# Optimization experiments

Measured on AMD Instinct MI355X. Metric: run time of the kernel, lower is better.

Reference implementation:

```python
import jax, jax.numpy as jnp
import numpy as np

KERNEL_SIZE = 32
KERNEL_STRIDE = 16
HEAD_NUM_K = 4
HEAD_DIM = 128
BATCH = 4
SEQ_LEN = 16384


def _calc_chunks_with_stride(cu_seqlens_np, chunk_size, stride):
    """Mirror of calc_chunks_with_stride using numpy (index computation on host).

    Returns flat gather indices (num_chunks*chunk_size,) and compressed
    cumulative sequence lengths (batch+1,).
    """
    cu = np.asarray(cu_seqlens_np, dtype=np.int64)
    batch_sizes = cu[1:] - cu[:-1]
    max_seq_len = int(batch_sizes.max())
    max_chunks = max((max_seq_len - chunk_size) // stride + 1, 0)
    offsets = np.arange(0, max_chunks * stride, stride, dtype=np.int64)  # (C,)
    seq_starts = cu[:-1]
    chunk_start = seq_starts[:, None] + offsets[None, :]            # (B, C)
    chunk_end = chunk_start + chunk_size
    valid = chunk_end <= (seq_starts[:, None] + batch_sizes[:, None])  # (B, C)
    valid_starts = chunk_start[valid]                               # (N,)
    inner = np.arange(chunk_size, dtype=np.int64)[None, :]          # (1, K)
    flat_idx = (valid_starts[:, None] + inner).reshape(-1)          # (N*K,)
    n_per_batch = valid.sum(axis=1)
    cu_comp = np.zeros(len(cu), dtype=np.int32)
    cu_comp[1:] = np.cumsum(n_per_batch)
    return flat_idx, cu_comp


def setup_inputs() -> dict:
    key = jax.random.key(0)
    k = jax.random.normal(key, (BATCH * SEQ_LEN, HEAD_NUM_K, HEAD_DIM), dtype=jnp.float32)
    cu_seqlens = jnp.arange(BATCH + 1, dtype=jnp.int32) * SEQ_LEN
    return {"k": k, "cu_seqlens": cu_seqlens}


def reference(k, cu_seqlens):
    # Index computation is data-dependent on concrete cu_seqlens (host-side).
    flat_idx, cu_comp = _calc_chunks_with_stride(np.asarray(cu_seqlens), KERNEL_SIZE, KERNEL_STRIDE)
    idx = jnp.asarray(flat_idx)
    # Gather overlapping chunks: (N*K, H, D) -> (N, K, H, D) -> mean over K.
    gathered = k[idx]
    gathered = gathered.reshape(-1, KERNEL_SIZE, HEAD_NUM_K, HEAD_DIM)
    compressed_k = gathered.mean(axis=1)
    return compressed_k, jnp.asarray(cu_comp)
```

## Files before the change

kernel.cpp:

```cpp
#include <hip/hip_runtime.h>

#define KSIZE   32
#define KSTRIDE 16
#define HK      4
#define HD      128
#define ROW     (HK * HD)
#define ROW4    (ROW / 4)
#define BATCH   4
#define SEQLEN  16384
#define CHUNKS_PER_BATCH ((SEQLEN - KSIZE) / KSTRIDE + 1)
#define TOTAL_CHUNKS     (BATCH * CHUNKS_PER_BATCH)

#define SPAN 8
#define BLOCKS_PER_BATCH ((CHUNKS_PER_BATCH + SPAN - 1) / SPAN)
#define TOTAL_BLOCKS     (BATCH * BLOCKS_PER_BATCH)

__device__ __forceinline__ float4 sum16(const float4* __restrict__ src,
                                        int row0, int t) {
    float4 a0 = make_float4(0.f, 0.f, 0.f, 0.f);
    float4 a1 = make_float4(0.f, 0.f, 0.f, 0.f);
    #pragma unroll
    for (int i = 0; i < 8; ++i) {
        float4 u = src[(long)(row0 + 2 * i)     * ROW4 + t];
        float4 v = src[(long)(row0 + 2 * i + 1) * ROW4 + t];
        a0.x += u.x; a0.y += u.y; a0.z += u.z; a0.w += u.w;
        a1.x += v.x; a1.y += v.y; a1.z += v.z; a1.w += v.w;
    }
    a0.x += a1.x; a0.y += a1.y; a0.z += a1.z; a0.w += a1.w;
    return a0;
}

__global__ __launch_bounds__(128)
void compress_k_fused(const float* __restrict__ k,
                      const int* __restrict__ cu_seqlens,
                      float* __restrict__ out,
                      float* __restrict__ tail) {
    const int blk = blockIdx.x;
    const int b   = blk / BLOCKS_PER_BATCH;
    const int cb  = blk - b * BLOCKS_PER_BATCH;
    const int c0  = cb * SPAN;
    const int gc  = (CHUNKS_PER_BATCH - c0 < SPAN) ? (CHUNKS_PER_BATCH - c0)
                                                   : SPAN;

    const long start_row = (long)cu_seqlens[b] + (long)c0 * KSTRIDE;
    const float4* __restrict__ src = (const float4*)(k + start_row * ROW);
    const int t = threadIdx.x;

    const float s = 1.0f / (float)KSIZE;
    float* outp = out + (long)(b * CHUNKS_PER_BATCH + c0) * ROW;

    float4 prev = sum16(src, 0, t);

    if (gc == SPAN) {
        #pragma unroll
        for (int g = 0; g < SPAN; ++g) {
            float4 cur = sum16(src, (g + 1) * KSTRIDE, t);
            float4 r = make_float4((prev.x + cur.x) * s,
                                   (prev.y + cur.y) * s,
                                   (prev.z + cur.z) * s,
                                   (prev.w + cur.w) * s);
            ((float4*)(outp + (long)g * ROW))[t] = r;
            prev = cur;
        }
    } else {
        for (int g = 0; g < gc; ++g) {
            float4 cur = sum16(src, (g + 1) * KSTRIDE, t);
            float4 r = make_float4((prev.x + cur.x) * s,
                                   (prev.y + cur.y) * s,
                                   (prev.z + cur.z) * s,
                                   (prev.w + cur.w) * s);
            ((float4*)(outp + (long)g * ROW))[t] = r;
            prev = cur;
        }
    }

    if (blk == 0 && t == 0) {
        int run = 0;
        tail[0] = 0.0f;
        #pragma unroll
        for (int i = 0; i < BATCH; ++i) {
            const int len = cu_seqlens[i + 1] - cu_seqlens[i];
            const int n = (len >= KSIZE) ? (len - KSIZE) / KSTRIDE + 1 : 0;
            run += n;
            tail[i + 1] = (float)run;
        }
    }
}

extern "C" void kernel_launch(void* const* d_in, const int* in_sizes, int n_in,
                              void* d_out, int out_size, void* d_ws, size_t ws_size,
                              hipStream_t stream) {
    const float* k          = (const float*)d_in[0];
    const int*   cu_seqlens = (const int*)d_in[1];
    float*       out        = (float*)d_out;
    float*       tail       = out + (long)TOTAL_CHUNKS * ROW;

    compress_k_fused<<<TOTAL_BLOCKS, 128, 0, stream>>>(k, cu_seqlens, out, tail);
}
```

Measured before the change: 191.2 us.

## Double-buffer half-window loads into LDS via async global_load_lds

New measurement: 194.7 us. Within noise of the previous version (+1.8%).

```diff
diff --git a/kernel.cpp b/kernel.cpp
--- a/kernel.cpp
+++ b/kernel.cpp
@@ -14,27 +14,18 @@
 #define SPAN 8
 #define BLOCKS_PER_BATCH ((CHUNKS_PER_BATCH + SPAN - 1) / SPAN)
 #define TOTAL_BLOCKS     (BATCH * BLOCKS_PER_BATCH)
+#define HWBYTES (KSTRIDE * ROW * 4)
 
-__device__ __forceinline__ float4 sum16(const float4* __restrict__ src,
-                                        int row0, int t) {
-    float4 a0 = make_float4(0.f, 0.f, 0.f, 0.f);
-    float4 a1 = make_float4(0.f, 0.f, 0.f, 0.f);
-    #pragma unroll
-    for (int i = 0; i < 8; ++i) {
-        float4 u = src[(long)(row0 + 2 * i)     * ROW4 + t];
-        float4 v = src[(long)(row0 + 2 * i + 1) * ROW4 + t];
-        a0.x += u.x; a0.y += u.y; a0.z += u.z; a0.w += u.w;
-        a1.x += v.x; a1.y += v.y; a1.z += v.z; a1.w += v.w;
-    }
-    a0.x += a1.x; a0.y += a1.y; a0.z += a1.z; a0.w += a1.w;
-    return a0;
-}
+typedef const void __attribute__((address_space(1))) GAS;
+typedef void __attribute__((address_space(3)))       LAS;
 
 __global__ __launch_bounds__(128)
 void compress_k_fused(const float* __restrict__ k,
                       const int* __restrict__ cu_seqlens,
                       float* __restrict__ out,
                       float* __restrict__ tail) {
+    __shared__ float4 buf[2][KSTRIDE * ROW4];
+
     const int blk = blockIdx.x;
     const int b   = blk / BLOCKS_PER_BATCH;
     const int cb  = blk - b * BLOCKS_PER_BATCH;
@@ -42,36 +33,56 @@
     const int gc  = (CHUNKS_PER_BATCH - c0 < SPAN) ? (CHUNKS_PER_BATCH - c0)
                                                    : SPAN;
 
-    const long start_row = (long)cu_seqlens[b] + (long)c0 * KSTRIDE;
-    const float4* __restrict__ src = (const float4*)(k + start_row * ROW);
-    const int t = threadIdx.x;
+    const int t    = threadIdx.x;
+    const int w    = t >> 6;
+    const int lane = t & 63;
+
+    const char* gbase = (const char*)(k +
+        ((long)cu_seqlens[b] + (long)c0 * KSTRIDE) * ROW);
+
+    auto stage = [&](int sel, int j) {
+        const char* g = gbase + (size_t)j * HWBYTES + (size_t)w * (HWBYTES / 2)
+                        + (size_t)lane * 16;
+        char* l = (char*)&buf[sel][0] + (size_t)w * (HWBYTES / 2);
+        #pragma unroll
+        for (int i = 0; i < 16; ++i)
+            __builtin_amdgcn_global_load_lds((GAS*)(g + i * 1024),
+                                             (LAS*)(l + i * 1024), 16, 0, 0);
+    };
+
+    stage(0, 0);
 
     const float s = 1.0f / (float)KSIZE;
     float* outp = out + (long)(b * CHUNKS_PER_BATCH + c0) * ROW;
+    float4 prev = make_float4(0.f, 0.f, 0.f, 0.f);
 
-    float4 prev = sum16(src, 0, t);
+    for (int j = 0; j <= gc; ++j) {
+        if (j < gc) stage((j + 1) & 1, j + 1);
+        __syncthreads();
 
-    if (gc == SPAN) {
+        const float4* __restrict__ B = buf[j & 1];
+        float4 a0 = make_float4(0.f, 0.f, 0.f, 0.f);
+        float4 a1 = make_float4(0.f, 0.f, 0.f, 0.f);
         #pragma unroll
-        for (int g = 0; g < SPAN; ++g) {
-            float4 cur = sum16(src, (g + 1) * KSTRIDE, t);
+        for (int r = 0; r < KSTRIDE; r += 2) {
+            float4 u = B[r * ROW4 + t];
+            float4 v = B[(r + 1) * ROW4 + t];
+            a0.x += u.x; a0.y += u.y; a0.z += u.z; a0.w += u.w;
+            a1.x += v.x; a1.y += v.y; a1.z += v.z; a1.w += v.w;
+        }
+        float4 cur = make_float4(a0.x + a1.x, a0.y + a1.y,
+                                 a0.z + a1.z, a0.w + a1.w);
+
+        if (j > 0) {
             float4 r = make_float4((prev.x + cur.x) * s,
                                    (prev.y + cur.y) * s,
                                    (prev.z + cur.z) * s,
                                    (prev.w + cur.w) * s);
-            ((float4*)(outp + (long)g * ROW))[t] = r;
-            prev = cur;
+            ((float4*)(outp + (long)(j - 1) * ROW))[t] = r;
         }
-    } else {
-        for (int g = 0; g < gc; ++g) {
-            float4 cur = sum16(src, (g + 1) * KSTRIDE, t);
-            float4 r = make_float4((prev.x + cur.x) * s,
-                                   (prev.y + cur.y) * s,
-                                   (prev.z + cur.z) * s,
-                                   (prev.w + cur.w) * s);
-            ((float4*)(outp + (long)g * ROW))[t] = r;
-            prev = cur;
-        }
+        prev = cur;
+
+        __syncthreads();
     }
 
     if (blk == 0 && t == 0) {
```

## Split compression into half-window sum pass and combine pass via workspace

Applied to the files above, without the earlier changes.

After: 195.6 us. 1.02x slower.

```diff
diff --git a/kernel.cpp b/kernel.cpp
--- a/kernel.cpp
+++ b/kernel.cpp
@@ -10,10 +10,72 @@
 #define SEQLEN  16384
 #define CHUNKS_PER_BATCH ((SEQLEN - KSIZE) / KSTRIDE + 1)
 #define TOTAL_CHUNKS     (BATCH * CHUNKS_PER_BATCH)
+#define HW_PER_BATCH     (SEQLEN / KSTRIDE)
+#define TOTAL_HW         (BATCH * HW_PER_BATCH)
+#define WS_FLOATS        ((size_t)TOTAL_HW * ROW)
+
+
+__global__ __launch_bounds__(128)
+void hw_sums(const float* __restrict__ k,
+             const int* __restrict__ cu_seqlens,
+             float* __restrict__ H) {
+    const int j  = blockIdx.x;
+    const int b  = j >> 10;
+    const int hw = j & (HW_PER_BATCH - 1);
+    const float4* __restrict__ src = (const float4*)
+        (k + ((long)cu_seqlens[b] + (long)hw * KSTRIDE) * ROW);
+    const int t = threadIdx.x;
+
+    float4 a0 = make_float4(0.f, 0.f, 0.f, 0.f);
+    float4 a1 = make_float4(0.f, 0.f, 0.f, 0.f);
+    #pragma unroll
+    for (int r = 0; r < KSTRIDE; r += 2) {
+        float4 u = src[(long)r * ROW4 + t];
+        float4 v = src[(long)(r + 1) * ROW4 + t];
+        a0.x += u.x; a0.y += u.y; a0.z += u.z; a0.w += u.w;
+        a1.x += v.x; a1.y += v.y; a1.z += v.z; a1.w += v.w;
+    }
+    float4 s = make_float4(a0.x + a1.x, a0.y + a1.y, a0.z + a1.z, a0.w + a1.w);
+    ((float4*)(H + (long)j * ROW))[t] = s;
+}
+
+__global__ __launch_bounds__(256)
+void hw_combine(const float* __restrict__ H,
+                const int* __restrict__ cu_seqlens,
+                float* __restrict__ out,
+                float* __restrict__ tail) {
+    const int idx = blockIdx.x * 256 + threadIdx.x;
+    if (idx < TOTAL_CHUNKS * ROW4) {
+        const int chunk = idx >> 7;
+        const int col   = idx & (ROW4 - 1);
+        const int b     = chunk / CHUNKS_PER_BATCH;
+        const int c     = chunk - b * CHUNKS_PER_BATCH;
+
+        const long h = ((long)(b * HW_PER_BATCH + c)) * ROW4 + col;
+        float4 u = ((const float4*)H)[h];
+        float4 v = ((const float4*)H)[h + ROW4];
+        const float s = 1.0f / (float)KSIZE;
+        float4 r = make_float4((u.x + v.x) * s, (u.y + v.y) * s,
+                               (u.z + v.z) * s, (u.w + v.w) * s);
+        ((float4*)out)[(long)chunk * ROW4 + col] = r;
+    }
+
+    if (idx == 0) {
+        int run = 0;
+        tail[0] = 0.0f;
+        #pragma unroll
+        for (int i = 0; i < BATCH; ++i) {
+            const int len = cu_seqlens[i + 1] - cu_seqlens[i];
+            const int n = (len >= KSIZE) ? (len - KSIZE) / KSTRIDE + 1 : 0;
+            run += n;
+            tail[i + 1] = (float)run;
+        }
+    }
+}
 
 #define SPAN 8
-#define BLOCKS_PER_BATCH ((CHUNKS_PER_BATCH + SPAN - 1) / SPAN)
-#define TOTAL_BLOCKS     (BATCH * BLOCKS_PER_BATCH)
+#define FB_BLOCKS_PER_BATCH ((CHUNKS_PER_BATCH + SPAN - 1) / SPAN)
+#define FB_TOTAL_BLOCKS     (BATCH * FB_BLOCKS_PER_BATCH)
 
 __device__ __forceinline__ float4 sum16(const float4* __restrict__ src,
                                         int row0, int t) {
@@ -31,49 +93,30 @@
 }
 
 __global__ __launch_bounds__(128)
-void compress_k_fused(const float* __restrict__ k,
-                      const int* __restrict__ cu_seqlens,
-                      float* __restrict__ out,
-                      float* __restrict__ tail) {
+void compress_k_fallback(const float* __restrict__ k,
+                         const int* __restrict__ cu_seqlens,
+                         float* __restrict__ out,
+                         float* __restrict__ tail) {
     const int blk = blockIdx.x;
-    const int b   = blk / BLOCKS_PER_BATCH;
-    const int cb  = blk - b * BLOCKS_PER_BATCH;
+    const int b   = blk / FB_BLOCKS_PER_BATCH;
+    const int cb  = blk - b * FB_BLOCKS_PER_BATCH;
     const int c0  = cb * SPAN;
     const int gc  = (CHUNKS_PER_BATCH - c0 < SPAN) ? (CHUNKS_PER_BATCH - c0)
                                                    : SPAN;
-
-    const long start_row = (long)cu_seqlens[b] + (long)c0 * KSTRIDE;
-    const float4* __restrict__ src = (const float4*)(k + start_row * ROW);
+    const float4* __restrict__ src = (const float4*)
+        (k + ((long)cu_seqlens[b] + (long)c0 * KSTRIDE) * ROW);
     const int t = threadIdx.x;
-
     const float s = 1.0f / (float)KSIZE;
     float* outp = out + (long)(b * CHUNKS_PER_BATCH + c0) * ROW;
 
     float4 prev = sum16(src, 0, t);
-
-    if (gc == SPAN) {
-        #pragma unroll
-        for (int g = 0; g < SPAN; ++g) {
-            float4 cur = sum16(src, (g + 1) * KSTRIDE, t);
-            float4 r = make_float4((prev.x + cur.x) * s,
-                                   (prev.y + cur.y) * s,
-                                   (prev.z + cur.z) * s,
-                                   (prev.w + cur.w) * s);
-            ((float4*)(outp + (long)g * ROW))[t] = r;
-            prev = cur;
-        }
-    } else {
-        for (int g = 0; g < gc; ++g) {
-            float4 cur = sum16(src, (g + 1) * KSTRIDE, t);
-            float4 r = make_float4((prev.x + cur.x) * s,
-                                   (prev.y + cur.y) * s,
-                                   (prev.z + cur.z) * s,
-                                   (prev.w + cur.w) * s);
-            ((float4*)(outp + (long)g * ROW))[t] = r;
-            prev = cur;
-        }
+    for (int g = 0; g < gc; ++g) {
+        float4 cur = sum16(src, (g + 1) * KSTRIDE, t);
+        float4 r = make_float4((prev.x + cur.x) * s, (prev.y + cur.y) * s,
+                               (prev.z + cur.z) * s, (prev.w + cur.w) * s);
+        ((float4*)(outp + (long)g * ROW))[t] = r;
+        prev = cur;
     }
-
     if (blk == 0 && t == 0) {
         int run = 0;
         tail[0] = 0.0f;
@@ -95,5 +138,14 @@
     float*       out        = (float*)d_out;
     float*       tail       = out + (long)TOTAL_CHUNKS * ROW;
 
-    compress_k_fused<<<TOTAL_BLOCKS, 128, 0, stream>>>(k, cu_seqlens, out, tail);
+    if (ws_size >= WS_FLOATS * sizeof(float) && d_ws != nullptr) {
+        float* H = (float*)d_ws;
+        hw_sums<<<TOTAL_HW, 128, 0, stream>>>(k, cu_seqlens, H);
+        const int p2_threads = TOTAL_CHUNKS * ROW4;
+        const int p2_blocks  = (p2_threads + 255) / 256;
+        hw_combine<<<p2_blocks, 256, 0, stream>>>(H, cu_seqlens, out, tail);
+    } else {
+        compress_k_fallback<<<FB_TOTAL_BLOCKS, 128, 0, stream>>>(
+            k, cu_seqlens, out, tail);
+    }
 }
```
